# Performance work log

Measured on AMD Instinct MI355X. Metric: run time of the kernel, lower is better.

The kernel has to match this reference:

```python
import jax, jax.numpy as jnp
import numpy as np

N, L, H = 64, 1024, 1024

def setup_inputs() -> dict:
    key = jax.random.key(0)
    ks = jax.random.split(key, 6)
    scale = 1.0 / np.sqrt(H)
    return {
        "decoder_hidden": jax.random.normal(ks[0], (N, H), dtype=jnp.float32),
        "encoder_hiddens": jax.random.normal(ks[1], (N, L, H), dtype=jnp.float32),
        "mask": jax.random.randint(ks[2], (N, L), 0, 2) > 0,  # True = PAD position
        "W_h": jax.random.normal(ks[3], (H, H), dtype=jnp.float32) * scale,
        "W_s": jax.random.normal(ks[4], (H, H), dtype=jnp.float32) * scale,
        "v": jax.random.normal(ks[5], (H,), dtype=jnp.float32) * scale,
    }

def reference(decoder_hidden, encoder_hiddens, mask, W_h, W_s, v):
    # score(h_t, h_s) = v^T tanh(W_h h_t + W_s h_s)
    # torch Linear: y = x @ W.T
    dh = decoder_hidden @ W_h.T                      # [N, H]
    eh = jnp.einsum('nlh,kh->nlk', encoder_hiddens, W_s)  # [N, L, H]
    score = jnp.tanh(dh[:, None, :] + eh) @ v        # [N, L]
    score = jnp.where(mask, -jnp.inf, score)
    attn_weights = jax.nn.softmax(score, axis=1)     # [N, L]
    context = jnp.einsum('nl,nlh->nh', attn_weights, encoder_hiddens)  # [N, H]
    return (context, attn_weights)
```

## Files before the change

### kernel.cpp

```cpp
#include <hip/hip_runtime.h>
#include <hip/hip_bf16.h>
#include <math.h>

#define N_  64
#define L_  1024
#define H_  1024
#define NL_ (N_ * L_)

typedef __attribute__((ext_vector_type(8))) short bf16x8;
typedef __attribute__((ext_vector_type(4))) float f32x4;
typedef unsigned short ushort_t;
typedef unsigned int uint_t;

__device__ inline ushort_t f32_to_bf16_rne(float f) {
    uint_t u = __float_as_uint(f);
    u += 0x7FFFu + ((u >> 16) & 1u);
    return (ushort_t)(u >> 16);
}

__global__ __launch_bounds__(256) void convert_bf16_kernel(const float* __restrict__ src,
                                                           ushort_t* __restrict__ dst,
                                                           size_t nvec8) {
    size_t stride = (size_t)gridDim.x * 256;
    for (size_t g = (size_t)blockIdx.x * 256 + threadIdx.x; g < nvec8; g += stride) {
        size_t i = g * 8;
        float4 a = *(const float4*)(src + i);
        float4 b = *(const float4*)(src + i + 4);
        union { bf16x8 v; ushort_t u[8]; } o;
        o.u[0] = f32_to_bf16_rne(a.x); o.u[1] = f32_to_bf16_rne(a.y);
        o.u[2] = f32_to_bf16_rne(a.z); o.u[3] = f32_to_bf16_rne(a.w);
        o.u[4] = f32_to_bf16_rne(b.x); o.u[5] = f32_to_bf16_rne(b.y);
        o.u[6] = f32_to_bf16_rne(b.z); o.u[7] = f32_to_bf16_rne(b.w);
        *(bf16x8*)(dst + i) = o.v;
    }
}

__global__ __launch_bounds__(256) void dh_kernel(const float* __restrict__ ddec,
                                                 const float* __restrict__ Wh,
                                                 float* __restrict__ dh) {
    int i = blockIdx.x * 256 + threadIdx.x;
    int n = i >> 10;
    const float* a = ddec + (size_t)n * H_;
    const float* w = Wh + (size_t)(i & (H_ - 1)) * H_;
    float acc = 0.f;
#pragma unroll 8
    for (int h = 0; h < H_; h += 4) {
        float4 av = *(const float4*)(a + h);
        float4 wv = *(const float4*)(w + h);
        acc += av.x * wv.x + av.y * wv.y + av.z * wv.z + av.w * wv.w;
    }
    dh[i] = acc;
}

__device__ inline void stage_tile(const ushort_t* __restrict__ gbase,
                                  ushort_t* lds, int tid, size_t row0_off) {
#pragma unroll
    for (int j = 0; j < 2; j++) {
        int c_lin = j * 256 + tid;
        int r  = c_lin >> 2;
        int cp = c_lin & 3;
        int q  = cp ^ ((r >> 1) & 3);
        const ushort_t* g = gbase + row0_off + (size_t)r * H_ + q * 8;
        ushort_t* l = lds + (size_t)(j * 256 + (tid & ~63)) * 8;
        __builtin_amdgcn_global_load_lds((const __attribute__((address_space(1))) void*)g,
                                         (__attribute__((address_space(3))) void*)l,
                                         16, 0, 0);
    }
}

__global__ __launch_bounds__(256) void score_mfma_kernel(const ushort_t* __restrict__ enc_bf,
                                                         const ushort_t* __restrict__ ws_bf,
                                                         const float* __restrict__ dh,
                                                         const float* __restrict__ v,
                                                         float* __restrict__ score) {
    __shared__ ushort_t As[128 * 32];
    __shared__ ushort_t Bs[128 * 32];

    const int b  = blockIdx.x;
    const int i0 = ((b & 7) | ((b >> 6) << 3)) * 128;
    const int k0 = ((b >> 3) & 7) * 128;
    const int tid  = threadIdx.x;
    const int lane = tid & 63;
    const int wv   = tid >> 6;
    const int wr   = (wv >> 1) * 64;
    const int wc   = (wv & 1) * 64;
    const int m    = lane & 15;
    const int q    = lane >> 4;
    const int qs   = q ^ ((m >> 1) & 3);

    f32x4 acc[4][4];
#pragma unroll
    for (int a = 0; a < 4; a++)
#pragma unroll
        for (int c = 0; c < 4; c++)
            acc[a][c] = (f32x4){0.f, 0.f, 0.f, 0.f};

    for (int h0 = 0; h0 < H_; h0 += 32) {
        __syncthreads();
        stage_tile(enc_bf, As, tid, (size_t)i0 * H_ + h0);
        stage_tile(ws_bf,  Bs, tid, (size_t)k0 * H_ + h0);
        __syncthreads();

        bf16x8 af[4], bfr[4];
#pragma unroll
        for (int ti = 0; ti < 4; ti++) {
            int r = wr + ti * 16 + m;
            af[ti] = *(const bf16x8*)(As + (size_t)(r * 4 + qs) * 8);
        }
#pragma unroll
        for (int tj = 0; tj < 4; tj++) {
            int r = wc + tj * 16 + m;
            bfr[tj] = *(const bf16x8*)(Bs + (size_t)(r * 4 + qs) * 8);
        }
#pragma unroll
        for (int ti = 0; ti < 4; ti++)
#pragma unroll
            for (int tj = 0; tj < 4; tj++)
                acc[ti][tj] = __builtin_amdgcn_mfma_f32_16x16x32_bf16(
                    af[ti], bfr[tj], acc[ti][tj], 0, 0, 0);
    }

    const int nb = i0 >> 10;
    float vv[4], dhv[4];
#pragma unroll
    for (int tj = 0; tj < 4; tj++) {
        int k = k0 + wc + tj * 16 + m;
        vv[tj]  = v[k];
        dhv[tj] = dh[nb * H_ + k];
    }
#pragma unroll
    for (int ti = 0; ti < 4; ti++) {
#pragma unroll
        for (int reg = 0; reg < 4; reg++) {
            float s = 0.f;
#pragma unroll
            for (int tj = 0; tj < 4; tj++) {
                float x  = dhv[tj] + acc[ti][tj][reg];
                float e2 = __expf(2.f * x);
                s += vv[tj] * (1.f - 2.f / (e2 + 1.f));
            }
            s += __shfl_xor(s, 1);
            s += __shfl_xor(s, 2);
            s += __shfl_xor(s, 4);
            s += __shfl_xor(s, 8);
            if (m == 0) {
                int i_local = wr + ti * 16 + q * 4 + reg;
                atomicAdd(&score[i0 + i_local], s);
            }
        }
    }
}

__global__ __launch_bounds__(256) void softmax_kernel(const float* __restrict__ score,
                                                      const int* __restrict__ mask,
                                                      float* __restrict__ attn) {
    const int n = blockIdx.x;
    const int t = threadIdx.x;
    __shared__ float redmax[4];
    __shared__ float redsum[4];

    float s[4];
    int   mk[4];
    float mymax = -INFINITY;
#pragma unroll
    for (int j = 0; j < 4; j++) {
        int l = t + j * 256;
        mk[j] = mask[n * L_ + l];
        s[j] = mk[j] ? -INFINITY : score[n * L_ + l];
        mymax = fmaxf(mymax, s[j]);
    }
#pragma unroll
    for (int off = 1; off < 64; off <<= 1)
        mymax = fmaxf(mymax, __shfl_xor(mymax, off));
    if ((t & 63) == 0) redmax[t >> 6] = mymax;
    __syncthreads();
    float gmax = fmaxf(fmaxf(redmax[0], redmax[1]), fmaxf(redmax[2], redmax[3]));

    float e[4];
    float mysum = 0.f;
#pragma unroll
    for (int j = 0; j < 4; j++) {
        e[j] = mk[j] ? 0.f : __expf(s[j] - gmax);
        mysum += e[j];
    }
#pragma unroll
    for (int off = 1; off < 64; off <<= 1)
        mysum += __shfl_xor(mysum, off);
    if ((t & 63) == 0) redsum[t >> 6] = mysum;
    __syncthreads();
    float gsum = redsum[0] + redsum[1] + redsum[2] + redsum[3];
    float inv = 1.f / gsum;
#pragma unroll
    for (int j = 0; j < 4; j++)
        attn[n * L_ + t + j * 256] = e[j] * inv;
}

__global__ __launch_bounds__(128) void context_partial_kernel(const ushort_t* __restrict__ enc_bf,
                                                              const float* __restrict__ attn,
                                                              float* __restrict__ cpart) {
    const int n  = blockIdx.x;
    const int lc = blockIdx.y;
    const int l0 = lc * 128;
    const int t  = threadIdx.x;
    const int h0 = t * 8;

    __shared__ float w[128];
    w[t] = attn[n * L_ + l0 + t];
    __syncthreads();

    const ushort_t* base = enc_bf + (size_t)n * L_ * H_ + (size_t)l0 * H_ + h0;
    float acc[8] = {};
#pragma unroll 4
    for (int l = 0; l < 128; l++) {
        union { bf16x8 v; ushort_t u[8]; } e;
        e.v = *(const bf16x8*)(base + (size_t)l * H_);
        float wl = w[l];
#pragma unroll
        for (int j = 0; j < 8; j++)
            acc[j] += wl * __uint_as_float(((uint_t)e.u[j]) << 16);
    }
    float* dst = cpart + ((size_t)lc * N_ + n) * H_ + h0;
    *(float4*)(dst + 0) = (float4){acc[0], acc[1], acc[2], acc[3]};
    *(float4*)(dst + 4) = (float4){acc[4], acc[5], acc[6], acc[7]};
}

__global__ __launch_bounds__(256) void context_reduce_kernel(const float* __restrict__ cpart,
                                                             float* __restrict__ ctx) {
    int i = blockIdx.x * 256 + threadIdx.x;
    float s = 0.f;
#pragma unroll
    for (int lc = 0; lc < 8; lc++)
        s += cpart[(size_t)lc * N_ * H_ + i];
    ctx[i] = s;
}

extern "C" void kernel_launch(void* const* d_in, const int* in_sizes, int n_in,
                              void* d_out, int out_size, void* d_ws, size_t ws_size,
                              hipStream_t stream) {
    const float* ddec = (const float*)d_in[0];
    const float* enc  = (const float*)d_in[1];
    const int*   mask = (const int*)d_in[2];
    const float* Wh   = (const float*)d_in[3];
    const float* Ws   = (const float*)d_in[4];
    const float* v    = (const float*)d_in[5];

    float* out_ctx  = (float*)d_out;
    float* out_attn = out_ctx + N_ * H_;

    ushort_t* enc_bf = (ushort_t*)d_ws;
    ushort_t* ws_bf  = enc_bf + (size_t)NL_ * H_;
    float*    dh     = (float*)(ws_bf + (size_t)H_ * H_);
    float*    score  = dh + N_ * H_;
    float*    cpart  = score + NL_;

    convert_bf16_kernel<<<4096, 256, 0, stream>>>(enc, enc_bf, (size_t)NL_ * H_ / 8);
    convert_bf16_kernel<<<512, 256, 0, stream>>>(Ws, ws_bf, (size_t)H_ * H_ / 8);

    hipMemsetAsync(score, 0, (size_t)NL_ * sizeof(float), stream);

    dh_kernel<<<NL_ / 256, 256, 0, stream>>>(ddec, Wh, dh);

    score_mfma_kernel<<<4096, 256, 0, stream>>>(enc_bf, ws_bf, dh, v, score);

    softmax_kernel<<<N_, 256, 0, stream>>>(score, mask, out_attn);

    dim3 g4(N_, 8);
    context_partial_kernel<<<g4, 128, 0, stream>>>(enc_bf, out_attn, cpart);
    context_reduce_kernel<<<NL_ / 1024 * 4, 256, 0, stream>>>(cpart, out_ctx);
}
```

Measured before the change: 646.1 us.

## Restructure score GEMM into 256x256 double-buffered pipelined MFMA kernel

```diff
diff --git a/kernel.cpp b/kernel.cpp
--- a/kernel.cpp
+++ b/kernel.cpp
@@ -6,6 +6,7 @@
 #define L_  1024
 #define H_  1024
 #define NL_ (N_ * L_)
+#define NT_ 16
 
 typedef __attribute__((ext_vector_type(8))) short bf16x8;
 typedef __attribute__((ext_vector_type(4))) float f32x4;
@@ -52,72 +53,153 @@
     dh[i] = acc;
 }
 
-__device__ inline void stage_tile(const ushort_t* __restrict__ gbase,
-                                  ushort_t* lds, int tid, size_t row0_off) {
-#pragma unroll
-    for (int j = 0; j < 2; j++) {
-        int c_lin = j * 256 + tid;
-        int r  = c_lin >> 2;
-        int cp = c_lin & 3;
-        int q  = cp ^ ((r >> 1) & 3);
-        const ushort_t* g = gbase + row0_off + (size_t)r * H_ + q * 8;
-        ushort_t* l = lds + (size_t)(j * 256 + (tid & ~63)) * 8;
-        __builtin_amdgcn_global_load_lds((const __attribute__((address_space(1))) void*)g,
-                                         (__attribute__((address_space(3))) void*)l,
-                                         16, 0, 0);
-    }
-}
-
-__global__ __launch_bounds__(256) void score_mfma_kernel(const ushort_t* __restrict__ enc_bf,
-                                                         const ushort_t* __restrict__ ws_bf,
-                                                         const float* __restrict__ dh,
-                                                         const float* __restrict__ v,
-                                                         float* __restrict__ score) {
-    __shared__ ushort_t As[128 * 32];
-    __shared__ ushort_t Bs[128 * 32];
+__device__ __forceinline__ void glds(const ushort_t* g, ushort_t* l) {
+    __builtin_amdgcn_global_load_lds((const __attribute__((address_space(1))) void*)g,
+                                     (__attribute__((address_space(3))) void*)l,
+                                     16, 0, 0);
+}
+
+__global__ __launch_bounds__(512, 2) void score_mfma_kernel(const ushort_t* __restrict__ enc_bf,
+                                                            const ushort_t* __restrict__ ws_bf,
+                                                            const float* __restrict__ dh,
+                                                            const float* __restrict__ v,
+                                                            float* __restrict__ score) {
+    __shared__ ushort_t lds[65536];
 
     const int b  = blockIdx.x;
-    const int i0 = ((b & 7) | ((b >> 6) << 3)) * 128;
-    const int k0 = ((b >> 3) & 7) * 128;
+    const int i0 = ((b & 7) | ((b >> 5) << 3)) << 8;
+    const int k0 = ((b >> 3) & 3) << 8;
     const int tid  = threadIdx.x;
     const int lane = tid & 63;
-    const int wv   = tid >> 6;
-    const int wr   = (wv >> 1) * 64;
-    const int wc   = (wv & 1) * 64;
+    const int w    = tid >> 6;
+    const int wr   = (w >> 2) << 7;
+    const int wc   = (w & 3) << 6;
     const int m    = lane & 15;
     const int q    = lane >> 4;
-    const int qs   = q ^ ((m >> 1) & 3);
-
-    f32x4 acc[4][4];
-#pragma unroll
-    for (int a = 0; a < 4; a++)
+    const int half = w >> 2;
+    const int grp  = w & 3;
+
+    const int g_lane = (lane >> 3) * H_ + (((lane & 7) ^ (lane >> 3)) << 3);
+    const int csw0 = ((q ^ (m & 7)) << 3);
+    const int csw1 = (((4 | q) ^ (m & 7)) << 3);
+
+    const int rA0 = (half << 7) + (grp << 5);
+    const int rB0 = (grp << 6) + (half << 4);
+
+    {
+        const ushort_t* gA = enc_bf + (size_t)i0 * H_ + g_lane;
+        const ushort_t* gB = ws_bf  + (size_t)k0 * H_ + g_lane;
+        ushort_t* An = lds;
+        ushort_t* Bn = lds + 32768;
+        glds(gA + (size_t)(rA0 +  0) * H_, An + (rA0 +  0) * 64);
+        glds(gA + (size_t)(rA0 +  8) * H_, An + (rA0 +  8) * 64);
+        glds(gA + (size_t)(rA0 + 16) * H_, An + (rA0 + 16) * 64);
+        glds(gA + (size_t)(rA0 + 24) * H_, An + (rA0 + 24) * 64);
+        glds(gB + (size_t)(rB0 +  0) * H_, Bn + (rB0 +  0) * 64);
+        glds(gB + (size_t)(rB0 +  8) * H_, Bn + (rB0 +  8) * 64);
+        glds(gB + (size_t)(rB0 + 32) * H_, Bn + (rB0 + 32) * 64);
+        glds(gB + (size_t)(rB0 + 40) * H_, Bn + (rB0 + 40) * 64);
+        asm volatile("s_waitcnt vmcnt(0)" ::: "memory");
+        __builtin_amdgcn_s_barrier();
+    }
+
+    f32x4 acc[8][4];
+#pragma unroll
+    for (int a = 0; a < 8; a++)
 #pragma unroll
         for (int c = 0; c < 4; c++)
             acc[a][c] = (f32x4){0.f, 0.f, 0.f, 0.f};
 
-    for (int h0 = 0; h0 < H_; h0 += 32) {
-        __syncthreads();
-        stage_tile(enc_bf, As, tid, (size_t)i0 * H_ + h0);
-        stage_tile(ws_bf,  Bs, tid, (size_t)k0 * H_ + h0);
-        __syncthreads();
-
-        bf16x8 af[4], bfr[4];
-#pragma unroll
-        for (int ti = 0; ti < 4; ti++) {
-            int r = wr + ti * 16 + m;
-            af[ti] = *(const bf16x8*)(As + (size_t)(r * 4 + qs) * 8);
-        }
-#pragma unroll
-        for (int tj = 0; tj < 4; tj++) {
-            int r = wc + tj * 16 + m;
-            bfr[tj] = *(const bf16x8*)(Bs + (size_t)(r * 4 + qs) * 8);
-        }
-#pragma unroll
-        for (int ti = 0; ti < 4; ti++)
-#pragma unroll
-            for (int tj = 0; tj < 4; tj++)
-                acc[ti][tj] = __builtin_amdgcn_mfma_f32_16x16x32_bf16(
-                    af[ti], bfr[tj], acc[ti][tj], 0, 0, 0);
+    const int rowA = wr + m;
+    const int rowB = wc + m;
+
+#pragma unroll 2
+    for (int kt = 0; kt < NT_; ++kt) {
+        ushort_t* Ac = lds + ((kt & 1) << 14);
+        ushort_t* Bc = lds + 32768 + ((kt & 1) << 14);
+        ushort_t* An = lds + (((kt + 1) & 1) << 14);
+        ushort_t* Bn = lds + 32768 + (((kt + 1) & 1) << 14);
+        const int h0n = ((kt + 1) & (NT_ - 1)) << 6;
+        const ushort_t* gA = enc_bf + (size_t)i0 * H_ + h0n + g_lane;
+        const ushort_t* gB = ws_bf  + (size_t)k0 * H_ + h0n + g_lane;
+
+        bf16x8 af[8], b0, b1, b2, b3;
+
+#pragma unroll
+        for (int ti = 0; ti < 8; ti++)
+            af[ti] = *(const bf16x8*)(Ac + (rowA + ti * 16) * 64 + csw0);
+        b0 = *(const bf16x8*)(Bc + (rowB +  0) * 64 + csw0);
+        b1 = *(const bf16x8*)(Bc + (rowB + 16) * 64 + csw0);
+        glds(gA + (size_t)(rA0 + 0) * H_, An + (rA0 + 0) * 64);
+        glds(gA + (size_t)(rA0 + 8) * H_, An + (rA0 + 8) * 64);
+        __builtin_amdgcn_s_barrier();
+        asm volatile("s_waitcnt lgkmcnt(0)" ::: "memory");
+        __builtin_amdgcn_sched_barrier(0);
+        __builtin_amdgcn_s_setprio(1);
+#pragma unroll
+        for (int ti = 0; ti < 8; ti++)
+            acc[ti][0] = __builtin_amdgcn_mfma_f32_16x16x32_bf16(af[ti], b0, acc[ti][0], 0, 0, 0);
+#pragma unroll
+        for (int ti = 0; ti < 8; ti++)
+            acc[ti][1] = __builtin_amdgcn_mfma_f32_16x16x32_bf16(af[ti], b1, acc[ti][1], 0, 0, 0);
+        __builtin_amdgcn_s_setprio(0);
+        asm volatile("s_waitcnt vmcnt(2)" ::: "memory");
+        __builtin_amdgcn_s_barrier();
+
+        b2 = *(const bf16x8*)(Bc + (rowB + 32) * 64 + csw0);
+        b3 = *(const bf16x8*)(Bc + (rowB + 48) * 64 + csw0);
+        glds(gA + (size_t)(rA0 + 16) * H_, An + (rA0 + 16) * 64);
+        glds(gA + (size_t)(rA0 + 24) * H_, An + (rA0 + 24) * 64);
+        __builtin_amdgcn_s_barrier();
+        asm volatile("s_waitcnt lgkmcnt(0)" ::: "memory");
+        __builtin_amdgcn_sched_barrier(0);
+        __builtin_amdgcn_s_setprio(1);
+#pragma unroll
+        for (int ti = 0; ti < 8; ti++)
+            acc[ti][2] = __builtin_amdgcn_mfma_f32_16x16x32_bf16(af[ti], b2, acc[ti][2], 0, 0, 0);
+#pragma unroll
+        for (int ti = 0; ti < 8; ti++)
+            acc[ti][3] = __builtin_amdgcn_mfma_f32_16x16x32_bf16(af[ti], b3, acc[ti][3], 0, 0, 0);
+        __builtin_amdgcn_s_setprio(0);
+        __builtin_amdgcn_s_barrier();
+
+#pragma unroll
+        for (int ti = 0; ti < 8; ti++)
+            af[ti] = *(const bf16x8*)(Ac + (rowA + ti * 16) * 64 + csw1);
+        b0 = *(const bf16x8*)(Bc + (rowB +  0) * 64 + csw1);
+        b1 = *(const bf16x8*)(Bc + (rowB + 16) * 64 + csw1);
+        glds(gB + (size_t)(rB0 + 0) * H_, Bn + (rB0 + 0) * 64);
+        glds(gB + (size_t)(rB0 + 8) * H_, Bn + (rB0 + 8) * 64);
+        __builtin_amdgcn_s_barrier();
+        asm volatile("s_waitcnt lgkmcnt(0)" ::: "memory");
+        __builtin_amdgcn_sched_barrier(0);
+        __builtin_amdgcn_s_setprio(1);
+#pragma unroll
+        for (int ti = 0; ti < 8; ti++)
+            acc[ti][0] = __builtin_amdgcn_mfma_f32_16x16x32_bf16(af[ti], b0, acc[ti][0], 0, 0, 0);
+#pragma unroll
+        for (int ti = 0; ti < 8; ti++)
+            acc[ti][1] = __builtin_amdgcn_mfma_f32_16x16x32_bf16(af[ti], b1, acc[ti][1], 0, 0, 0);
+        __builtin_amdgcn_s_setprio(0);
+        __builtin_amdgcn_s_barrier();
+
+        b2 = *(const bf16x8*)(Bc + (rowB + 32) * 64 + csw1);
+        b3 = *(const bf16x8*)(Bc + (rowB + 48) * 64 + csw1);
+        glds(gB + (size_t)(rB0 + 32) * H_, Bn + (rB0 + 32) * 64);
+        glds(gB + (size_t)(rB0 + 40) * H_, Bn + (rB0 + 40) * 64);
+        __builtin_amdgcn_s_barrier();
+        asm volatile("s_waitcnt lgkmcnt(0)" ::: "memory");
+        __builtin_amdgcn_sched_barrier(0);
+        __builtin_amdgcn_s_setprio(1);
+#pragma unroll
+        for (int ti = 0; ti < 8; ti++)
+            acc[ti][2] = __builtin_amdgcn_mfma_f32_16x16x32_bf16(af[ti], b2, acc[ti][2], 0, 0, 0);
+#pragma unroll
+        for (int ti = 0; ti < 8; ti++)
+            acc[ti][3] = __builtin_amdgcn_mfma_f32_16x16x32_bf16(af[ti], b3, acc[ti][3], 0, 0, 0);
+        __builtin_amdgcn_s_setprio(0);
+        asm volatile("s_waitcnt vmcnt(2)" ::: "memory");
+        __builtin_amdgcn_s_barrier();
     }
 
     const int nb = i0 >> 10;
@@ -129,7 +211,7 @@
         dhv[tj] = dh[nb * H_ + k];
     }
 #pragma unroll
-    for (int ti = 0; ti < 4; ti++) {
+    for (int ti = 0; ti < 8; ti++) {
 #pragma unroll
         for (int reg = 0; reg < 4; reg++) {
             float s = 0.f;
@@ -260,7 +342,7 @@
 
     dh_kernel<<<NL_ / 256, 256, 0, stream>>>(ddec, Wh, dh);
 
-    score_mfma_kernel<<<4096, 256, 0, stream>>>(enc_bf, ws_bf, dh, v, score);
+    score_mfma_kernel<<<1024, 512, 0, stream>>>(enc_bf, ws_bf, dh, v, score);
 
     softmax_kernel<<<N_, 256, 0, stream>>>(score, mask, out_attn);
 
```

After: 607.0 us. 1.06x faster.
